# Kernel tuning notes

Hardware: AMD Instinct MI355X
Metric: run time of the kernel (lower is better)

The kernel has to match this reference:

```python
import jax, jax.numpy as jnp
import numpy as np
import jax.lax as lax

H, D, C, CS, NS, OW, PD = 8, 64, 512, 64, 5, 8, 1
MAX_LR = 0.1
KCONV = 4


def short_conv(x, w, b):
    # x: (B,T,Din) -> causal depthwise conv over time
    B, T, Din = x.shape
    xc = jnp.transpose(x, (0, 2, 1))
    xc = jnp.pad(xc, ((0, 0), (0, 0), (KCONV - 1, 0)))
    xc = lax.conv_general_dilated(xc, w, window_strides=(1,), padding='VALID',
                                  dimension_numbers=('NCW', 'OIW', 'NCW'),
                                  feature_group_count=Din)
    xc = xc + b[:, jnp.newaxis]
    return jnp.transpose(xc, (0, 2, 1))


def linear_scan(h_init, gates, inputs):
    # h_t = gate_t * h_{t-1} + input_t ; gates: (B,cs,H), inputs: (B,cs,H,...)
    extra = inputs.ndim - gates.ndim
    g = gates.reshape(gates.shape + (1,) * extra)
    first = g[:, 0:1] * h_init[:, jnp.newaxis] + inputs[:, 0:1]
    mod_in = jnp.concatenate([first, inputs[:, 1:]], axis=1)
    mod_g = jnp.concatenate([jnp.zeros_like(g[:, 0:1]), g[:, 1:]], axis=1)

    def assoc(a, bb):
        ga, xa = a
        gb, xb = bb
        return (ga * gb, gb * xa + xb)

    _, h_all = lax.associative_scan(assoc, (mod_g, mod_in), axis=1)
    return h_all, h_all[:, -1]


def omega_aggregate(u, gamma, w):
    cs = u.shape[1]
    cum = jnp.cumsum(gamma * u, axis=1)
    if w >= cs:
        return cum
    shifted = jnp.concatenate([jnp.zeros_like(cum[:, :w]), cum[:, :-w]], axis=1)
    return cum - shifted


def polar_express(S, steps):
    # Newton-Schulz quintic orthogonalization (Muon/Polar-Express coefficients)
    a, b, c = 3.4445, -4.7750, 2.0315
    n = jnp.sqrt(jnp.sum(S * S, axis=(-2, -1), keepdims=True))
    X = S / (n * 1.01 + 1e-7)
    for _ in range(steps):
        A = X @ jnp.swapaxes(X, -2, -1)
        X = a * X + (b * A + c * (A @ A)) @ X
    return X


def rms_norm(x):
    ms = jnp.mean(x * x, axis=-1, keepdims=True)
    return x * lax.rsqrt(ms + 1e-6)


def atlas_forward(x, Wq, Wk, Wv, Wproj, conv_q_w, conv_q_b, conv_k_w, conv_k_b,
                  conv_v_w, conv_v_b, ga_w, ga_b, ge_w, ge_b, gt_w, gt_b,
                  gg_w, gg_b, poly_coeffs, ln_gamma, W1_init, rg_w):
    B, T, _ = x.shape
    q = short_conv(x @ Wq.T, conv_q_w, conv_q_b).reshape(B, T, H, D)
    k = short_conv(x @ Wk.T, conv_k_w, conv_k_b).reshape(B, T, H, D)
    v = short_conv(x @ Wv.T, conv_v_w, conv_v_b).reshape(B, T, H, D)

    def phi(z):
        r = poly_coeffs[0] * z
        zp = z
        for i in range(1, PD):
            zp = zp * z
            r = r + poly_coeffs[i] * zp
        return r

    q, k = phi(q), phi(k)

    alpha = jax.nn.sigmoid(x @ ga_w.T + ga_b)          # (B,T,H) memory retention
    eta = MAX_LR * jax.nn.sigmoid(x @ ge_w.T + ge_b)   # learning rate
    theta = jax.nn.sigmoid(x @ gt_w.T + gt_b)          # momentum decay
    gamma = jax.nn.sigmoid(x @ gg_w.T + gg_b)          # omega context gate

    nC = T // CS

    def chunk(z):
        return jnp.moveaxis(z.reshape(B, nC, CS, *z.shape[2:]), 1, 0)

    q_ch, k_ch, v_ch = chunk(q), chunk(k), chunk(v)
    a_ch = chunk(alpha)[..., None]
    e_ch = chunk(eta)[..., None]
    t_ch = chunk(theta)[..., None]
    g_ch = chunk(gamma)[..., None]

    M0 = jnp.broadcast_to(W1_init, (B, H, D, D))
    S0 = jnp.zeros((B, H, D, D), x.dtype)

    def step(carry, inp):
        M, S = carry
        q_c, k_c, v_c, a_c, e_c, t_c, g_c = inp
        pred = jnp.einsum('bhvk,bchk->bchv', M, k_c)
        err = pred - v_c
        u = (2.0 / D) * jnp.einsum('bchv,bchk->bchvk', err, k_c)
        u = omega_aggregate(u, g_c[..., None], OW)
        mom_in = -(e_c[..., None] * u)
        chunk_S, S = linear_scan(S, jnp.squeeze(t_c, -1), mom_in)
        chunk_S_orth = polar_express(chunk_S, NS)
        M_all, M = linear_scan(M, jnp.squeeze(a_c, -1), chunk_S_orth)
        y_c = jnp.einsum('bchvk,bchk->bchv', M_all, q_c)
        return (M, S), y_c

    (_, _), y = lax.scan(step, (M0, S0), (q_ch, k_ch, v_ch, a_ch, e_ch, t_ch, g_ch))
    y = jnp.moveaxis(y, 0, 1).reshape(B, T, H, D)
    y = rms_norm(y) * (1.0 + ln_gamma)
    rg = jax.nn.sigmoid(x @ rg_w.T)          # (B,T,H) retrieve gate
    y = y * rg[..., None]
    return y.reshape(B, T, H * D) @ Wproj.T


def setup_inputs() -> dict:
    key = jax.random.key(0)
    ks = jax.random.split(key, 24)
    B, T = 2, 1024
    Din = H * D

    def lin(k, o, i):
        return jax.random.normal(k, (o, i), jnp.float32) * (1.0 / np.sqrt(i))

    bound = float(np.sqrt(6.0 / (D + D)))
    return dict(
        x=jax.random.normal(ks[0], (B, T, C), jnp.float32),
        Wq=lin(ks[1], Din, C), Wk=lin(ks[2], Din, C), Wv=lin(ks[3], Din, C),
        Wproj=lin(ks[4], C, Din),
        conv_q_w=jax.random.normal(ks[5], (Din, 1, KCONV), jnp.float32) * 0.02,
        conv_q_b=jnp.zeros(Din, jnp.float32),
        conv_k_w=jax.random.normal(ks[6], (Din, 1, KCONV), jnp.float32) * 0.02,
        conv_k_b=jnp.zeros(Din, jnp.float32),
        conv_v_w=jax.random.normal(ks[7], (Din, 1, KCONV), jnp.float32) * 0.02,
        conv_v_b=jnp.zeros(Din, jnp.float32),
        ga_w=lin(ks[8], H, C), ga_b=jnp.zeros(H, jnp.float32),
        ge_w=lin(ks[9], H, C), ge_b=jnp.zeros(H, jnp.float32),
        gt_w=lin(ks[10], H, C), gt_b=jnp.zeros(H, jnp.float32),
        gg_w=lin(ks[11], H, C), gg_b=jnp.zeros(H, jnp.float32),
        poly_coeffs=jnp.ones(PD, jnp.float32),
        ln_gamma=jnp.zeros((H, D), jnp.float32),
        W1_init=jax.random.uniform(ks[12], (H, D, D), jnp.float32, -bound, bound),
        rg_w=lin(ks[13], H, C),
    )


def reference(x, Wq, Wk, Wv, Wproj, conv_q_w, conv_q_b, conv_k_w, conv_k_b,
              conv_v_w, conv_v_b, ga_w, ga_b, ge_w, ge_b, gt_w, gt_b,
              gg_w, gg_b, poly_coeffs, ln_gamma, W1_init, rg_w):
    return atlas_forward(x, Wq, Wk, Wv, Wproj, conv_q_w, conv_q_b, conv_k_w,
                         conv_k_b, conv_v_w, conv_v_b, ga_w, ga_b, ge_w, ge_b,
                         gt_w, gt_b, gg_w, gg_b, poly_coeffs, ln_gamma,
                         W1_init, rg_w)
```

## Files before the change

### kernel.cpp

```cpp
#include <hip/hip_runtime.h>

#define B_ 2
#define T_ 1024
#define H_ 8
#define D_ 64
#define PPAD 68

typedef __attribute__((ext_vector_type(8))) short s8v;
typedef __attribute__((ext_vector_type(4))) short s4v;
typedef __attribute__((ext_vector_type(4))) float f4v;

__device__ __forceinline__ short f2bf(float f) {
  unsigned u = __float_as_uint(f);
  u += 0x7fffu + ((u >> 16) & 1u);
  return (short)(u >> 16);
}
__device__ __forceinline__ float bf2f(short s) {
  return __uint_as_float(((unsigned)(unsigned short)s) << 16);
}
__device__ __forceinline__ float sigm(float v) { return 1.0f / (1.0f + __expf(-v)); }

#define MFMA(a, b, c) __builtin_amdgcn_mfma_f32_16x16x32_bf16((a), (b), (c), 0, 0, 0)

__global__ __launch_bounds__(256) void gemm_bt(const float* __restrict__ A,
    const float* __restrict__ Bw, float* __restrict__ Co,
    int M, int N, int K) {
  __shared__ short Ash[64][40], Asl[64][40];
  __shared__ short Bsh[64][40], Bsl[64][40];
  const int tid = threadIdx.x;
  const int lane = tid & 63;
  const int wv = tid >> 6;
  const int wr = (wv >> 1) * 32;
  const int wc = (wv & 1) * 32;
  const int m0 = blockIdx.x * 64;
  const int n0 = blockIdx.y * 64;
  const int ldr = tid >> 2;
  const int ldc = (tid & 3) * 8;
  const int l15 = lane & 15;
  const int kq = (lane >> 4) * 8;
  f4v acc[2][2];
#pragma unroll
  for (int i = 0; i < 2; ++i)
#pragma unroll
    for (int j = 0; j < 2; ++j)
#pragma unroll
      for (int r = 0; r < 4; ++r) acc[i][j][r] = 0.0f;
  const float* ap = A + (size_t)(m0 + ldr) * K + ldc;
  const float* bp = Bw + (size_t)(n0 + ldr) * K + ldc;
  for (int kt = 0; kt < K; kt += 32) {
    float4 av0 = *(const float4*)(ap + kt);
    float4 av1 = *(const float4*)(ap + kt + 4);
    float4 bv0 = *(const float4*)(bp + kt);
    float4 bv1 = *(const float4*)(bp + kt + 4);
    float af[8] = {av0.x, av0.y, av0.z, av0.w, av1.x, av1.y, av1.z, av1.w};
    float bf[8] = {bv0.x, bv0.y, bv0.z, bv0.w, bv1.x, bv1.y, bv1.z, bv1.w};
    s8v ah, al, bh, bl;
#pragma unroll
    for (int i = 0; i < 8; ++i) {
      short h = f2bf(af[i]); ah[i] = h; al[i] = f2bf(af[i] - bf2f(h));
      h = f2bf(bf[i]); bh[i] = h; bl[i] = f2bf(bf[i] - bf2f(h));
    }
    __syncthreads();
    *(s8v*)&Ash[ldr][ldc] = ah; *(s8v*)&Asl[ldr][ldc] = al;
    *(s8v*)&Bsh[ldr][ldc] = bh; *(s8v*)&Bsl[ldr][ldc] = bl;
    __syncthreads();
    s8v a0h = *(const s8v*)&Ash[wr + l15][kq];
    s8v a1h = *(const s8v*)&Ash[wr + 16 + l15][kq];
    s8v b0h = *(const s8v*)&Bsh[wc + l15][kq];
    s8v b1h = *(const s8v*)&Bsh[wc + 16 + l15][kq];
    s8v a0l = *(const s8v*)&Asl[wr + l15][kq];
    s8v a1l = *(const s8v*)&Asl[wr + 16 + l15][kq];
    s8v b0l = *(const s8v*)&Bsl[wc + l15][kq];
    s8v b1l = *(const s8v*)&Bsl[wc + 16 + l15][kq];
    acc[0][0] = MFMA(a0h, b0h, acc[0][0]);
    acc[0][1] = MFMA(a0h, b1h, acc[0][1]);
    acc[1][0] = MFMA(a1h, b0h, acc[1][0]);
    acc[1][1] = MFMA(a1h, b1h, acc[1][1]);
    acc[0][0] = MFMA(a0h, b0l, acc[0][0]);
    acc[0][1] = MFMA(a0h, b1l, acc[0][1]);
    acc[1][0] = MFMA(a1h, b0l, acc[1][0]);
    acc[1][1] = MFMA(a1h, b1l, acc[1][1]);
    acc[0][0] = MFMA(a0l, b0h, acc[0][0]);
    acc[0][1] = MFMA(a0l, b1h, acc[0][1]);
    acc[1][0] = MFMA(a1l, b0h, acc[1][0]);
    acc[1][1] = MFMA(a1l, b1h, acc[1][1]);
  }
#pragma unroll
  for (int m2 = 0; m2 < 2; ++m2)
#pragma unroll
    for (int n2 = 0; n2 < 2; ++n2)
#pragma unroll
      for (int r = 0; r < 4; ++r) {
        int row = m0 + wr + m2 * 16 + (lane >> 4) * 4 + r;
        int col = n0 + wc + n2 * 16 + l15;
        Co[(size_t)row * N + col] = acc[m2][n2][r];
      }
}

__global__ __launch_bounds__(256) void gemm_qkv(const float* __restrict__ A,
    const float* __restrict__ Wq, const float* __restrict__ Wk,
    const float* __restrict__ Wv,
    float* __restrict__ xq, float* __restrict__ xk, float* __restrict__ xv) {
  __shared__ short Ash[64][40], Asl[64][40];
  __shared__ short Bsh[64][40], Bsl[64][40];
  const int sel = blockIdx.y >> 3;
  const float* Bw = sel == 0 ? Wq : (sel == 1 ? Wk : Wv);
  float* Co = sel == 0 ? xq : (sel == 1 ? xk : xv);
  const int tid = threadIdx.x;
  const int lane = tid & 63;
  const int wv = tid >> 6;
  const int wr = (wv >> 1) * 32;
  const int wc = (wv & 1) * 32;
  const int m0 = blockIdx.x * 64;
  const int n0 = (blockIdx.y & 7) * 64;
  const int ldr = tid >> 2;
  const int ldc = (tid & 3) * 8;
  const int l15 = lane & 15;
  const int kq = (lane >> 4) * 8;
  f4v acc[2][2];
#pragma unroll
  for (int i = 0; i < 2; ++i)
#pragma unroll
    for (int j = 0; j < 2; ++j)
#pragma unroll
      for (int r = 0; r < 4; ++r) acc[i][j][r] = 0.0f;
  const float* ap = A + (size_t)(m0 + ldr) * 512 + ldc;
  const float* bp = Bw + (size_t)(n0 + ldr) * 512 + ldc;
  for (int kt = 0; kt < 512; kt += 32) {
    float4 av0 = *(const float4*)(ap + kt);
    float4 av1 = *(const float4*)(ap + kt + 4);
    float4 bv0 = *(const float4*)(bp + kt);
    float4 bv1 = *(const float4*)(bp + kt + 4);
    float af[8] = {av0.x, av0.y, av0.z, av0.w, av1.x, av1.y, av1.z, av1.w};
    float bf[8] = {bv0.x, bv0.y, bv0.z, bv0.w, bv1.x, bv1.y, bv1.z, bv1.w};
    s8v ah, al, bh, bl;
#pragma unroll
    for (int i = 0; i < 8; ++i) {
      short h = f2bf(af[i]); ah[i] = h; al[i] = f2bf(af[i] - bf2f(h));
      h = f2bf(bf[i]); bh[i] = h; bl[i] = f2bf(bf[i] - bf2f(h));
    }
    __syncthreads();
    *(s8v*)&Ash[ldr][ldc] = ah; *(s8v*)&Asl[ldr][ldc] = al;
    *(s8v*)&Bsh[ldr][ldc] = bh; *(s8v*)&Bsl[ldr][ldc] = bl;
    __syncthreads();
    s8v a0h = *(const s8v*)&Ash[wr + l15][kq];
    s8v a1h = *(const s8v*)&Ash[wr + 16 + l15][kq];
    s8v b0h = *(const s8v*)&Bsh[wc + l15][kq];
    s8v b1h = *(const s8v*)&Bsh[wc + 16 + l15][kq];
    s8v a0l = *(const s8v*)&Asl[wr + l15][kq];
    s8v a1l = *(const s8v*)&Asl[wr + 16 + l15][kq];
    s8v b0l = *(const s8v*)&Bsl[wc + l15][kq];
    s8v b1l = *(const s8v*)&Bsl[wc + 16 + l15][kq];
    acc[0][0] = MFMA(a0h, b0h, acc[0][0]);
    acc[0][1] = MFMA(a0h, b1h, acc[0][1]);
    acc[1][0] = MFMA(a1h, b0h, acc[1][0]);
    acc[1][1] = MFMA(a1h, b1h, acc[1][1]);
    acc[0][0] = MFMA(a0h, b0l, acc[0][0]);
    acc[0][1] = MFMA(a0h, b1l, acc[0][1]);
    acc[1][0] = MFMA(a1h, b0l, acc[1][0]);
    acc[1][1] = MFMA(a1h, b1l, acc[1][1]);
    acc[0][0] = MFMA(a0l, b0h, acc[0][0]);
    acc[0][1] = MFMA(a0l, b1h, acc[0][1]);
    acc[1][0] = MFMA(a1l, b0h, acc[1][0]);
    acc[1][1] = MFMA(a1l, b1h, acc[1][1]);
  }
#pragma unroll
  for (int m2 = 0; m2 < 2; ++m2)
#pragma unroll
    for (int n2 = 0; n2 < 2; ++n2)
#pragma unroll
      for (int r = 0; r < 4; ++r) {
        int row = m0 + wr + m2 * 16 + (lane >> 4) * 4 + r;
        int col = n0 + wc + n2 * 16 + l15;
        Co[(size_t)row * 512 + col] = acc[m2][n2][r];
      }
}

__global__ __launch_bounds__(256) void conv3_k(
    const float* __restrict__ xq, const float* __restrict__ xk,
    const float* __restrict__ xv,
    const float* __restrict__ cqw, const float* __restrict__ cqb,
    const float* __restrict__ ckw, const float* __restrict__ ckb,
    const float* __restrict__ cvw, const float* __restrict__ cvb,
    const float* __restrict__ pc,
    float* __restrict__ qb, float* __restrict__ kb, float* __restrict__ vb) {
  const int s = blockIdx.x >> 12;
  const int idx = ((blockIdx.x & 4095) << 8) + threadIdx.x;
  const float* in = s == 0 ? xq : (s == 1 ? xk : xv);
  const float* w  = s == 0 ? cqw : (s == 1 ? ckw : cvw);
  const float* bs = s == 0 ? cqb : (s == 1 ? ckb : cvb);
  float* o        = s == 0 ? qb : (s == 1 ? kb : vb);
  const int d = idx & 511;
  const int bt = idx >> 9;
  const int t = bt & (T_ - 1);
  float acc = bs[d];
#pragma unroll
  for (int j = 0; j < 4; ++j) {
    int tt = t - 3 + j;
    if (tt >= 0) acc += w[d * 4 + j] * in[(size_t)(bt - 3 + j) * 512 + d];
  }
  float sc = (s < 2) ? pc[0] : 1.0f;
  o[idx] = sc * acc;
}

__global__ __launch_bounds__(256) void gates_k(const float* __restrict__ x,
    const float* __restrict__ gaw, const float* __restrict__ gab,
    const float* __restrict__ gew, const float* __restrict__ geb,
    const float* __restrict__ gtw, const float* __restrict__ gtb,
    const float* __restrict__ ggw, const float* __restrict__ ggb,
    const float* __restrict__ rgw,
    float* __restrict__ alpha, float* __restrict__ eta,
    float* __restrict__ theta, float* __restrict__ gam, float* __restrict__ rg) {
  int wv = threadIdx.x >> 6, lane = threadIdx.x & 63;
  int bt = blockIdx.x * 4 + wv;
  float xr[8];
#pragma unroll
  for (int i = 0; i < 8; ++i) xr[i] = x[(size_t)bt * 512 + i * 64 + lane];
  for (int h = 0; h < 8; ++h) {
    float s0 = 0, s1 = 0, s2 = 0, s3 = 0, s4 = 0;
#pragma unroll
    for (int i = 0; i < 8; ++i) {
      float xv = xr[i];
      int o = h * 512 + i * 64 + lane;
      s0 += xv * gaw[o];
      s1 += xv * gew[o];
      s2 += xv * gtw[o];
      s3 += xv * ggw[o];
      s4 += xv * rgw[o];
    }
#pragma unroll
    for (int off = 32; off >= 1; off >>= 1) {
      s0 += __shfl_xor(s0, off);
      s1 += __shfl_xor(s1, off);
      s2 += __shfl_xor(s2, off);
      s3 += __shfl_xor(s3, off);
      s4 += __shfl_xor(s4, off);
    }
    if (lane == 0) {
      size_t o = (size_t)bt * 8 + h;
      alpha[o] = sigm(s0 + gab[h]);
      eta[o]   = 0.1f * sigm(s1 + geb[h]);
      theta[o] = sigm(s2 + gtb[h]);
      gam[o]   = sigm(s3 + ggb[h]);
      rg[o]    = sigm(s4);
    }
  }
}

__global__ __launch_bounds__(256) void init_carry(const float* __restrict__ w1,
    float* __restrict__ Mc, float* __restrict__ Sc) {
  int idx = blockIdx.x * 256 + threadIdx.x;
  Mc[idx] = w1[idx & 32767];
  Sc[idx] = 0.0f;
}

__global__ __launch_bounds__(256) void chunk_a(
    const float* __restrict__ kb, const float* __restrict__ vb,
    const float* __restrict__ eta, const float* __restrict__ theta,
    const float* __restrict__ gam,
    const float* __restrict__ Mc, float* __restrict__ Sc,
    float* __restrict__ chS, int ci) {
  __shared__ float KT[64][65];
  __shared__ float errl[4][68];
  __shared__ float Ml[4][64];
  __shared__ float ge_[64], gt_[64], gg_[64];
  const int tid = threadIdx.x;
  const int bh = blockIdx.x >> 4;
  const int vs = blockIdx.x & 15;
  const int b = bh >> 3, h = bh & 7;
  const int v0 = vs * 4;
  const int t0 = ci * 64;
  const int lane = tid & 63, q4 = tid >> 6;
  for (int it = 0; it < 16; ++it) {
    int c = it * 4 + q4;
    KT[lane][c] = kb[((size_t)(b * T_ + t0 + c) * H_ + h) * 64 + lane];
  }
  if (tid < 64) {
    size_t gi = (size_t)(b * T_ + t0 + tid) * H_ + h;
    ge_[tid] = eta[gi]; gt_[tid] = theta[gi]; gg_[tid] = gam[gi];
  }
  Ml[q4][lane] = Mc[((size_t)bh * 64 + v0 + q4) * 64 + lane];
  __syncthreads();
  {
    int c = lane, vr = q4;
    float p = 0.0f;
#pragma unroll
    for (int k2 = 0; k2 < 64; ++k2) p += KT[k2][c] * Ml[vr][k2];
    float vv = vb[((size_t)(b * T_ + t0 + c) * H_ + h) * 64 + v0 + vr];
    errl[vr][c] = p - vv;
  }
  __syncthreads();
  {
    const int kk = lane, vr = q4, v = v0 + vr;
    float S = Sc[((size_t)bh * 64 + v) * 64 + kk];
    float ring[8];
    float cum = 0.0f;
    float* out = chS + ((size_t)(b << 6) * 8 + h) * 4096 + (size_t)v * 64 + kk;
    for (int c8 = 0; c8 < 8; ++c8) {
#pragma unroll
      for (int j = 0; j < 8; ++j) {
        int c = c8 * 8 + j;
        float u = 0.03125f * errl[vr][c] * KT[kk][c];
        float gu = gg_[c] * u;
        cum += gu;
        if (c8 > 0) cum -= ring[j];
        ring[j] = gu;
        float mom = -ge_[c] * cum;
        S = gt_[c] * S + mom;
        out[(size_t)c * 32768] = S;
      }
    }
    Sc[((size_t)bh * 64 + v) * 64 + kk] = S;
  }
}

__device__ __forceinline__ s8v ld8(const short* p) {
  s4v lo = *(const s4v*)p;
  s4v hi = *(const s4v*)(p + 4);
  s8v r;
  r[0] = lo[0]; r[1] = lo[1]; r[2] = lo[2]; r[3] = lo[3];
  r[4] = hi[0]; r[5] = hi[1]; r[6] = hi[2]; r[7] = hi[3];
  return r;
}

__device__ __forceinline__ void mm4(const short (*Ah)[PPAD], const short (*Al)[PPAD],
    const short (*Bh)[PPAD], const short (*Bl)[PPAD],
    int wr, int wc, int l15, int kq, int sp, f4v acc[2][2]) {
#pragma unroll
  for (int kt = 0; kt < 64; kt += 32) {
    s8v a0h = ld8(&Ah[wr + l15][kt + kq]);
    s8v a1h = ld8(&Ah[wr + 16 + l15][kt + kq]);
    s8v b0h = ld8(&Bh[wc + l15][kt + kq]);
    s8v b1h = ld8(&Bh[wc + 16 + l15][kt + kq]);
    acc[0][0] = MFMA(a0h, b0h, acc[0][0]);
    acc[0][1] = MFMA(a0h, b1h, acc[0][1]);
    acc[1][0] = MFMA(a1h, b0h, acc[1][0]);
    acc[1][1] = MFMA(a1h, b1h, acc[1][1]);
    if (sp) {
      s8v a0l = ld8(&Al[wr + l15][kt + kq]);
      s8v a1l = ld8(&Al[wr + 16 + l15][kt + kq]);
      s8v b0l = ld8(&Bl[wc + l15][kt + kq]);
      s8v b1l = ld8(&Bl[wc + 16 + l15][kt + kq]);
      acc[0][0] = MFMA(a0h, b0l, acc[0][0]);
      acc[0][1] = MFMA(a0h, b1l, acc[0][1]);
      acc[1][0] = MFMA(a1h, b0l, acc[1][0]);
      acc[1][1] = MFMA(a1h, b1l, acc[1][1]);
      acc[0][0] = MFMA(a0l, b0h, acc[0][0]);
      acc[0][1] = MFMA(a0l, b1h, acc[0][1]);
      acc[1][0] = MFMA(a1l, b0h, acc[1][0]);
      acc[1][1] = MFMA(a1l, b1h, acc[1][1]);
    }
  }
}

__global__ __launch_bounds__(256, 3) void polar_k(float* __restrict__ cs) {
  __shared__ short Xh[64][PPAD], Xl[64][PPAD];
  __shared__ short XTh[64][PPAD], XTl[64][PPAD];
  __shared__ short Zh[64][PPAD], Zl[64][PPAD];
  __shared__ float red[4];
  const int tid = threadIdx.x;
  const int lane = tid & 63;
  const int w = tid >> 6;
  const int wr = (w >> 1) * 32;
  const int wc = (w & 1) * 32;
  const int l15 = lane & 15;
  const int q4 = lane >> 4;
  const int kq = q4 * 8;
  float* base = cs + (size_t)blockIdx.x * 4096;
  float xr[2][2][4];
  float ss = 0.0f;
#pragma unroll
  for (int m2 = 0; m2 < 2; ++m2)
#pragma unroll
    for (int n2 = 0; n2 < 2; ++n2)
#pragma unroll
      for (int r = 0; r < 4; ++r) {
        float v = base[(wr + m2 * 16 + q4 * 4 + r) * 64 + wc + n2 * 16 + l15];
        xr[m2][n2][r] = v;
        ss += v * v;
      }
#pragma unroll
  for (int off = 32; off >= 1; off >>= 1) ss += __shfl_xor(ss, off);
  if (lane == 0) red[w] = ss;
  __syncthreads();
  float scale = 1.0f / (sqrtf(red[0] + red[1] + red[2] + red[3]) * 1.01f + 1e-7f);
#pragma unroll
  for (int m2 = 0; m2 < 2; ++m2)
#pragma unroll
    for (int n2 = 0; n2 < 2; ++n2) {
      const int rr0 = wr + m2 * 16 + q4 * 4;
      const int cc = wc + n2 * 16 + l15;
      s4v hv, lv;
#pragma unroll
      for (int r = 0; r < 4; ++r) {
        float xv = xr[m2][n2][r] * scale;
        xr[m2][n2][r] = xv;
        short hh = f2bf(xv);
        short ll = f2bf(xv - bf2f(hh));
        hv[r] = hh; lv[r] = ll;
        Xh[rr0 + r][cc] = hh;
        Xl[rr0 + r][cc] = ll;
      }
      *(s4v*)&XTh[cc][rr0] = hv;
      *(s4v*)&XTl[cc][rr0] = lv;
    }
  __syncthreads();

  for (int it = 0; it < 5; ++it) {
    const int sp = (it < 4);
    f4v at[2][2];
#pragma unroll
    for (int m2 = 0; m2 < 2; ++m2)
#pragma unroll
      for (int n2 = 0; n2 < 2; ++n2)
#pragma unroll
        for (int r = 0; r < 4; ++r) at[m2][n2][r] = 0.0f;
    mm4(XTh, XTl, XTh, XTl, wr, wc, l15, kq, sp, at);
#pragma unroll
    for (int m2 = 0; m2 < 2; ++m2)
#pragma unroll
      for (int n2 = 0; n2 < 2; ++n2) {
        const int rr0 = wr + m2 * 16 + q4 * 4;
        const int cc = wc + n2 * 16 + l15;
        s4v hv, lv;
#pragma unroll
        for (int r = 0; r < 4; ++r) {
          float a = at[m2][n2][r];
          short hh = f2bf(a);
          hv[r] = hh; lv[r] = f2bf(a - bf2f(hh));
        }
        *(s4v*)&Zh[cc][rr0] = hv;
        if (sp) *(s4v*)&Zl[cc][rr0] = lv;
      }
    __syncthreads();
    f4v a2[2][2];
#pragma unroll
    for (int m2 = 0; m2 < 2; ++m2)
#pragma unroll
      for (int n2 = 0; n2 < 2; ++n2)
#pragma unroll
        for (int r = 0; r < 4; ++r) a2[m2][n2][r] = 0.0f;
    mm4(Zh, Zl, Zh, Zl, wr, wc, l15, kq, sp, a2);
    float zt[2][2][4];
#pragma unroll
    for (int m2 = 0; m2 < 2; ++m2)
#pragma unroll
      for (int n2 = 0; n2 < 2; ++n2)
#pragma unroll
        for (int r = 0; r < 4; ++r)
          zt[m2][n2][r] = -4.7750f * at[m2][n2][r] + 2.0315f * a2[m2][n2][r];
    __syncthreads();
#pragma unroll
    for (int m2 = 0; m2 < 2; ++m2)
#pragma unroll
      for (int n2 = 0; n2 < 2; ++n2) {
        const int rr0 = wr + m2 * 16 + q4 * 4;
        const int cc = wc + n2 * 16 + l15;
        s4v hv, lv;
#pragma unroll
        for (int r = 0; r < 4; ++r) {
          float zv = zt[m2][n2][r];
          short hh = f2bf(zv);
          hv[r] = hh; lv[r] = f2bf(zv - bf2f(hh));
        }
        *(s4v*)&Zh[cc][rr0] = hv;
        if (sp) *(s4v*)&Zl[cc][rr0] = lv;
      }
    __syncthreads();
    f4v q3[2][2];
#pragma unroll
    for (int m2 = 0; m2 < 2; ++m2)
#pragma unroll
      for (int n2 = 0; n2 < 2; ++n2)
#pragma unroll
        for (int r = 0; r < 4; ++r) q3[m2][n2][r] = 0.0f;
    mm4(Xh, Xl, Zh, Zl, wr, wc, l15, kq, sp, q3);
#pragma unroll
    for (int m2 = 0; m2 < 2; ++m2)
#pragma unroll
      for (int n2 = 0; n2 < 2; ++n2)
#pragma unroll
        for (int r = 0; r < 4; ++r)
          xr[m2][n2][r] = 3.4445f * xr[m2][n2][r] + q3[m2][n2][r];
    if (it < 4) {
      __syncthreads();
      const int slo = (it < 3);
#pragma unroll
      for (int m2 = 0; m2 < 2; ++m2)
#pragma unroll
        for (int n2 = 0; n2 < 2; ++n2) {
          const int rr0 = wr + m2 * 16 + q4 * 4;
          const int cc = wc + n2 * 16 + l15;
          s4v hv, lv;
#pragma unroll
          for (int r = 0; r < 4; ++r) {
            float xv = xr[m2][n2][r];
            short hh = f2bf(xv);
            short ll = f2bf(xv - bf2f(hh));
            hv[r] = hh; lv[r] = ll;
            Xh[rr0 + r][cc] = hh;
            if (slo) Xl[rr0 + r][cc] = ll;
          }
          *(s4v*)&XTh[cc][rr0] = hv;
          if (slo) *(s4v*)&XTl[cc][rr0] = lv;
        }
      __syncthreads();
    }
  }
#pragma unroll
  for (int m2 = 0; m2 < 2; ++m2)
#pragma unroll
    for (int n2 = 0; n2 < 2; ++n2)
#pragma unroll
      for (int r = 0; r < 4; ++r)
        base[(wr + m2 * 16 + q4 * 4 + r) * 64 + wc + n2 * 16 + l15] = xr[m2][n2][r];
}

__global__ __launch_bounds__(256, 1) void chunk_ca(
    const float* __restrict__ qb, const float* __restrict__ kb,
    const float* __restrict__ vb,
    const float* __restrict__ alpha, const float* __restrict__ eta,
    const float* __restrict__ theta, const float* __restrict__ gam,
    float* __restrict__ Mc, float* __restrict__ Sc,
    float* __restrict__ chS, float* __restrict__ yb, int ci) {
  __shared__ float KT[64][65];
  __shared__ float errl[4][68];
  __shared__ float Ml[4][64];
  __shared__ float ge_[64], gt_[64], gg_[64];
  const int tid = threadIdx.x, lane = tid & 63, w = tid >> 6;
  const int bh = blockIdx.x >> 4, vs = blockIdx.x & 15;
  const int b = bh >> 3, h = bh & 7;
  const int v0 = vs * 4, v = v0 + w;
  const int t0 = ci * 64;
  float M = Mc[((size_t)bh * 64 + v) * 64 + lane];
  const float* op = chS + ((size_t)(b << 6) * 8 + h) * 4096 + (size_t)v * 64 + lane;
  const float* qp = qb + ((size_t)(b * T_ + t0) * 8 + h) * 64 + lane;
  float* yp = yb + ((size_t)(b * T_ + t0) * 8 + h) * 64 + v;
  float av = alpha[(size_t)(b * T_ + t0 + lane) * 8 + h];
  float ov[64], qv[64];
#pragma unroll
  for (int c = 0; c < 64; ++c) ov[c] = op[(size_t)c * 32768];
#pragma unroll
  for (int c = 0; c < 64; ++c) qv[c] = qp[(size_t)c * 512];
#pragma unroll
  for (int c = 0; c < 64; ++c) {
    M = __builtin_fmaf(__shfl(av, c), M, ov[c]);
    float p = M * qv[c];
#pragma unroll
    for (int off = 32; off >= 1; off >>= 1) p += __shfl_xor(p, off);
    if (lane == 0) yp[(size_t)c * 512] = p;
  }
  Mc[((size_t)bh * 64 + v) * 64 + lane] = M;
  if (ci == 15) return;
  const int t1 = t0 + 64;
  Ml[w][lane] = M;
  for (int it = 0; it < 16; ++it) {
    int c = it * 4 + w;
    KT[lane][c] = kb[((size_t)(b * T_ + t1 + c) * 8 + h) * 64 + lane];
  }
  if (tid < 64) {
    size_t gi = (size_t)(b * T_ + t1 + tid) * 8 + h;
    ge_[tid] = eta[gi]; gt_[tid] = theta[gi]; gg_[tid] = gam[gi];
  }
  __syncthreads();
  {
    int c = lane, vr = w;
    float pr = 0.0f;
#pragma unroll
    for (int k2 = 0; k2 < 64; ++k2) pr += KT[k2][c] * Ml[vr][k2];
    float vv = vb[((size_t)(b * T_ + t1 + c) * 8 + h) * 64 + v0 + vr];
    errl[vr][c] = pr - vv;
  }
  __syncthreads();
  {
    const int kk = lane, vr = w, vv2 = v0 + vr;
    float S = Sc[((size_t)bh * 64 + vv2) * 64 + kk];
    float ring[8];
    float cum = 0.0f;
    float* out = chS + ((size_t)(b << 6) * 8 + h) * 4096 + (size_t)vv2 * 64 + kk;
    for (int c8 = 0; c8 < 8; ++c8) {
#pragma unroll
      for (int j = 0; j < 8; ++j) {
        int c = c8 * 8 + j;
        float u = 0.03125f * errl[vr][c] * KT[kk][c];
        float gu = gg_[c] * u;
        cum += gu;
        if (c8 > 0) cum -= ring[j];
        ring[j] = gu;
        float mom = -ge_[c] * cum;
        S = gt_[c] * S + mom;
        out[(size_t)c * 32768] = S;
      }
    }
    Sc[((size_t)bh * 64 + vv2) * 64 + kk] = S;
  }
}

__global__ __launch_bounds__(256) void norm_k(const float* __restrict__ yb,
    const float* __restrict__ lng, const float* __restrict__ rg,
    float* __restrict__ yn) {
  const int lane = threadIdx.x & 63;
  const int gw = blockIdx.x * 4 + (threadIdx.x >> 6);
  const int h = gw & 7;
  const int bt = gw >> 3;
  float y = yb[(size_t)gw * 64 + lane];
  float s = y * y;
#pragma unroll
  for (int off = 32; off >= 1; off >>= 1) s += __shfl_xor(s, off);
  float r = rsqrtf(s * (1.0f / 64.0f) + 1e-6f);
  yn[(size_t)gw * 64 + lane] = y * r * (1.0f + lng[h * 64 + lane]) * rg[(size_t)bt * 8 + h];
}

extern "C" void kernel_launch(void* const* d_in, const int* in_sizes, int n_in,
                              void* d_out, int out_size, void* d_ws, size_t ws_size,
                              hipStream_t stream) {
  (void)in_sizes; (void)n_in; (void)out_size; (void)ws_size;
  const float* x   = (const float*)d_in[0];
  const float* Wq  = (const float*)d_in[1];
  const float* Wk  = (const float*)d_in[2];
  const float* Wv  = (const float*)d_in[3];
  const float* Wpr = (const float*)d_in[4];
  const float* cqw = (const float*)d_in[5];
  const float* cqb = (const float*)d_in[6];
  const float* ckw = (const float*)d_in[7];
  const float* ckb = (const float*)d_in[8];
  const float* cvw = (const float*)d_in[9];
  const float* cvb = (const float*)d_in[10];
  const float* gaw = (const float*)d_in[11];
  const float* gab = (const float*)d_in[12];
  const float* gew = (const float*)d_in[13];
  const float* geb = (const float*)d_in[14];
  const float* gtw = (const float*)d_in[15];
  const float* gtb = (const float*)d_in[16];
  const float* ggw = (const float*)d_in[17];
  const float* ggb = (const float*)d_in[18];
  const float* pc  = (const float*)d_in[19];
  const float* lng = (const float*)d_in[20];
  const float* w1  = (const float*)d_in[21];
  const float* rgw = (const float*)d_in[22];
  float* outp = (float*)d_out;

  float* chS = (float*)d_ws;
  float* xq = chS;
  float* xk = chS + 1048576;
  float* xv = chS + 2 * 1048576;
  float* yn = chS;
  char* wp = (char*)d_ws + (size_t)16 * 1024 * 1024;
  auto alloc = [&](size_t bytes) {
    char* p = wp;
    wp += (bytes + 255) & ~(size_t)255;
    return p;
  };
  const size_t BT = (size_t)B_ * T_;
  float* qb = (float*)alloc(BT * 512 * 4);
  float* kb = (float*)alloc(BT * 512 * 4);
  float* vb = (float*)alloc(BT * 512 * 4);
  float* yb = (float*)alloc(BT * 512 * 4);
  float* alpha = (float*)alloc(BT * 8 * 4);
  float* eta   = (float*)alloc(BT * 8 * 4);
  float* theta = (float*)alloc(BT * 8 * 4);
  float* gam   = (float*)alloc(BT * 8 * 4);
  float* rg    = (float*)alloc(BT * 8 * 4);
  float* Mc = (float*)alloc((size_t)65536 * 4);
  float* Sc = (float*)alloc((size_t)65536 * 4);

  init_carry<<<dim3(256), dim3(256), 0, stream>>>(w1, Mc, Sc);
  gemm_qkv<<<dim3(32, 24), dim3(256), 0, stream>>>(x, Wq, Wk, Wv, xq, xk, xv);
  conv3_k<<<dim3(12288), dim3(256), 0, stream>>>(xq, xk, xv, cqw, cqb, ckw, ckb,
                                                 cvw, cvb, pc, qb, kb, vb);
  gates_k<<<dim3(512), dim3(256), 0, stream>>>(x, gaw, gab, gew, geb, gtw, gtb,
                                               ggw, ggb, rgw, alpha, eta, theta, gam, rg);
  chunk_a<<<dim3(256), dim3(256), 0, stream>>>(kb, vb, eta, theta, gam, Mc, Sc, chS, 0);
  for (int ci = 0; ci < 16; ++ci) {
    polar_k<<<dim3(1024), dim3(256), 0, stream>>>(chS);
    chunk_ca<<<dim3(256), dim3(256), 0, stream>>>(qb, kb, vb, alpha, eta, theta, gam,
                                                  Mc, Sc, chS, yb, ci);
  }
  norm_k<<<dim3(4096), dim3(256), 0, stream>>>(yb, lng, rg, yn);
  gemm_bt<<<dim3(32, 8), dim3(256), 0, stream>>>(yn, Wpr, outp, 2048, 512, 512);
}
```

Measured before the change: 1.258 ms.

## Swizzle polar LDS tiles and restructure chunk_ca reductions for ILP

```diff
diff --git a/kernel.cpp b/kernel.cpp
--- a/kernel.cpp
+++ b/kernel.cpp
@@ -4,7 +4,7 @@
 #define T_ 1024
 #define H_ 8
 #define D_ 64
-#define PPAD 68
+#define SW(r, c) ((c) ^ (((r) & 7) << 3))
 
 typedef __attribute__((ext_vector_type(8))) short s8v;
 typedef __attribute__((ext_vector_type(4))) short s4v;
@@ -314,33 +314,26 @@
   }
 }
 
-__device__ __forceinline__ s8v ld8(const short* p) {
-  s4v lo = *(const s4v*)p;
-  s4v hi = *(const s4v*)(p + 4);
-  s8v r;
-  r[0] = lo[0]; r[1] = lo[1]; r[2] = lo[2]; r[3] = lo[3];
-  r[4] = hi[0]; r[5] = hi[1]; r[6] = hi[2]; r[7] = hi[3];
-  return r;
-}
-
-__device__ __forceinline__ void mm4(const short (*Ah)[PPAD], const short (*Al)[PPAD],
-    const short (*Bh)[PPAD], const short (*Bl)[PPAD],
+__device__ __forceinline__ void mm4(const short (*Ah)[64], const short (*Al)[64],
+    const short (*Bh)[64], const short (*Bl)[64],
     int wr, int wc, int l15, int kq, int sp, f4v acc[2][2]) {
 #pragma unroll
   for (int kt = 0; kt < 64; kt += 32) {
-    s8v a0h = ld8(&Ah[wr + l15][kt + kq]);
-    s8v a1h = ld8(&Ah[wr + 16 + l15][kt + kq]);
-    s8v b0h = ld8(&Bh[wc + l15][kt + kq]);
-    s8v b1h = ld8(&Bh[wc + 16 + l15][kt + kq]);
+    const int ra0 = wr + l15, ra1 = wr + 16 + l15;
+    const int rb0 = wc + l15, rb1 = wc + 16 + l15;
+    s8v a0h = *(const s8v*)&Ah[ra0][SW(ra0, kt + kq)];
+    s8v a1h = *(const s8v*)&Ah[ra1][SW(ra1, kt + kq)];
+    s8v b0h = *(const s8v*)&Bh[rb0][SW(rb0, kt + kq)];
+    s8v b1h = *(const s8v*)&Bh[rb1][SW(rb1, kt + kq)];
     acc[0][0] = MFMA(a0h, b0h, acc[0][0]);
     acc[0][1] = MFMA(a0h, b1h, acc[0][1]);
     acc[1][0] = MFMA(a1h, b0h, acc[1][0]);
     acc[1][1] = MFMA(a1h, b1h, acc[1][1]);
     if (sp) {
-      s8v a0l = ld8(&Al[wr + l15][kt + kq]);
-      s8v a1l = ld8(&Al[wr + 16 + l15][kt + kq]);
-      s8v b0l = ld8(&Bl[wc + l15][kt + kq]);
-      s8v b1l = ld8(&Bl[wc + 16 + l15][kt + kq]);
+      s8v a0l = *(const s8v*)&Al[ra0][SW(ra0, kt + kq)];
+      s8v a1l = *(const s8v*)&Al[ra1][SW(ra1, kt + kq)];
+      s8v b0l = *(const s8v*)&Bl[rb0][SW(rb0, kt + kq)];
+      s8v b1l = *(const s8v*)&Bl[rb1][SW(rb1, kt + kq)];
       acc[0][0] = MFMA(a0h, b0l, acc[0][0]);
       acc[0][1] = MFMA(a0h, b1l, acc[0][1]);
       acc[1][0] = MFMA(a1h, b0l, acc[1][0]);
@@ -354,9 +347,9 @@
 }
 
 __global__ __launch_bounds__(256, 3) void polar_k(float* __restrict__ cs) {
-  __shared__ short Xh[64][PPAD], Xl[64][PPAD];
-  __shared__ short XTh[64][PPAD], XTl[64][PPAD];
-  __shared__ short Zh[64][PPAD], Zl[64][PPAD];
+  __shared__ short Xh[64][64], Xl[64][64];
+  __shared__ short XTh[64][64], XTl[64][64];
+  __shared__ short Zh[64][64], Zl[64][64];
   __shared__ float red[4];
   const int tid = threadIdx.x;
   const int lane = tid & 63;
@@ -398,11 +391,11 @@
         short hh = f2bf(xv);
         short ll = f2bf(xv - bf2f(hh));
         hv[r] = hh; lv[r] = ll;
-        Xh[rr0 + r][cc] = hh;
-        Xl[rr0 + r][cc] = ll;
-      }
-      *(s4v*)&XTh[cc][rr0] = hv;
-      *(s4v*)&XTl[cc][rr0] = lv;
+        Xh[rr0 + r][SW(rr0 + r, cc)] = hh;
+        Xl[rr0 + r][SW(rr0 + r, cc)] = ll;
+      }
+      *(s4v*)&XTh[cc][SW(cc, rr0)] = hv;
+      *(s4v*)&XTl[cc][SW(cc, rr0)] = lv;
     }
   __syncthreads();
 
@@ -429,8 +422,8 @@
           short hh = f2bf(a);
           hv[r] = hh; lv[r] = f2bf(a - bf2f(hh));
         }
-        *(s4v*)&Zh[cc][rr0] = hv;
-        if (sp) *(s4v*)&Zl[cc][rr0] = lv;
+        *(s4v*)&Zh[cc][SW(cc, rr0)] = hv;
+        if (sp) *(s4v*)&Zl[cc][SW(cc, rr0)] = lv;
       }
     __syncthreads();
     f4v a2[2][2];
@@ -463,8 +456,8 @@
           short hh = f2bf(zv);
           hv[r] = hh; lv[r] = f2bf(zv - bf2f(hh));
         }
-        *(s4v*)&Zh[cc][rr0] = hv;
-        if (sp) *(s4v*)&Zl[cc][rr0] = lv;
+        *(s4v*)&Zh[cc][SW(cc, rr0)] = hv;
+        if (sp) *(s4v*)&Zl[cc][SW(cc, rr0)] = lv;
       }
     __syncthreads();
     f4v q3[2][2];
@@ -498,11 +491,11 @@
             short hh = f2bf(xv);
             short ll = f2bf(xv - bf2f(hh));
             hv[r] = hh; lv[r] = ll;
-            Xh[rr0 + r][cc] = hh;
-            if (slo) Xl[rr0 + r][cc] = ll;
+            Xh[rr0 + r][SW(rr0 + r, cc)] = hh;
+            if (slo) Xl[rr0 + r][SW(rr0 + r, cc)] = ll;
           }
-          *(s4v*)&XTh[cc][rr0] = hv;
-          if (slo) *(s4v*)&XTl[cc][rr0] = lv;
+          *(s4v*)&XTh[cc][SW(cc, rr0)] = hv;
+          if (slo) *(s4v*)&XTl[cc][SW(cc, rr0)] = lv;
         }
       __syncthreads();
     }
@@ -537,18 +530,28 @@
   const float* qp = qb + ((size_t)(b * T_ + t0) * 8 + h) * 64 + lane;
   float* yp = yb + ((size_t)(b * T_ + t0) * 8 + h) * 64 + v;
   float av = alpha[(size_t)(b * T_ + t0 + lane) * 8 + h];
-  float ov[64], qv[64];
-#pragma unroll
-  for (int c = 0; c < 64; ++c) ov[c] = op[(size_t)c * 32768];
-#pragma unroll
-  for (int c = 0; c < 64; ++c) qv[c] = qp[(size_t)c * 512];
-#pragma unroll
-  for (int c = 0; c < 64; ++c) {
-    M = __builtin_fmaf(__shfl(av, c), M, ov[c]);
-    float p = M * qv[c];
-#pragma unroll
-    for (int off = 32; off >= 1; off >>= 1) p += __shfl_xor(p, off);
-    if (lane == 0) yp[(size_t)c * 512] = p;
+#pragma unroll
+  for (int half = 0; half < 2; ++half) {
+    const int cb = half * 32;
+    float ov[32], qv[32], p[32];
+#pragma unroll
+    for (int j = 0; j < 32; ++j) ov[j] = op[(size_t)(cb + j) * 32768];
+#pragma unroll
+    for (int j = 0; j < 32; ++j) qv[j] = qp[(size_t)(cb + j) * 512];
+#pragma unroll
+    for (int j = 0; j < 32; ++j) {
+      M = __builtin_fmaf(__shfl(av, cb + j), M, ov[j]);
+      p[j] = M * qv[j];
+    }
+#pragma unroll
+    for (int j = 0; j < 32; ++j) {
+#pragma unroll
+      for (int off = 32; off >= 1; off >>= 1) p[j] += __shfl_xor(p[j], off);
+    }
+    if (lane == 0) {
+#pragma unroll
+      for (int j = 0; j < 32; ++j) yp[(size_t)(cb + j) * 512] = p[j];
+    }
   }
   Mc[((size_t)bh * 64 + v) * 64 + lane] = M;
   if (ci == 15) return;
@@ -565,11 +568,16 @@
   __syncthreads();
   {
     int c = lane, vr = w;
-    float pr = 0.0f;
-#pragma unroll
-    for (int k2 = 0; k2 < 64; ++k2) pr += KT[k2][c] * Ml[vr][k2];
+    float s0 = 0, s1 = 0, s2 = 0, s3 = 0;
+#pragma unroll
+    for (int k2 = 0; k2 < 64; k2 += 4) {
+      s0 += KT[k2 + 0][c] * Ml[vr][k2 + 0];
+      s1 += KT[k2 + 1][c] * Ml[vr][k2 + 1];
+      s2 += KT[k2 + 2][c] * Ml[vr][k2 + 2];
+      s3 += KT[k2 + 3][c] * Ml[vr][k2 + 3];
+    }
     float vv = vb[((size_t)(b * T_ + t1 + c) * 8 + h) * 64 + v0 + vr];
-    errl[vr][c] = pr - vv;
+    errl[vr][c] = (s0 + s1) + (s2 + s3) - vv;
   }
   __syncthreads();
   {
```

Measured after the change: 1.033 ms. 1.22x faster.
